# Kernel optimization log

Hardware: AMD Instinct MI355X
Metric: run time of the kernel (lower is better)

## Reference

```python
import jax, jax.numpy as jnp
import numpy as np

MARGIN = 0.1
PD_EPS = 1e-6  # torch.nn.PairwiseDistance default eps (added to the difference)

B = 4096
D = 512


def setup_inputs() -> dict:
    key = jax.random.key(0)
    k1, k2, k3 = jax.random.split(key, 3)
    return {
        "feature_ts": jax.random.normal(k1, (B, D), dtype=jnp.float32),
        "feature_image1": jax.random.normal(k2, (B, D), dtype=jnp.float32),
        "feature_image2": jax.random.normal(k3, (B, D), dtype=jnp.float32),
    }


def _safe_sqrt(sq):
    # sqrt with zero gradient at 0 (matches torch.cdist backward at zero distance)
    pos = sq > 0
    return jnp.where(pos, jnp.sqrt(jnp.where(pos, sq, 1.0)), 0.0)


def reference(feature_ts, feature_image1, feature_image2):
    b, d = feature_ts.shape
    # representations: [3B, D]
    reps = jnp.concatenate([feature_ts, feature_image1, feature_image2], axis=0)

    # cdist(feature_ts, reps, p=2) -> [B, 3B] via Gram-matrix expansion
    sq = (
        jnp.sum(feature_ts * feature_ts, axis=1)[:, None]
        + jnp.sum(reps * reps, axis=1)[None, :]
        - 2.0 * (feature_ts @ reps.T)
    )
    dist = _safe_sqrt(jnp.maximum(sq, 0.0))          # [B, 3B]
    dist = jax.nn.relu(dist)                          # faithful (no-op: dist >= 0)

    # PairwiseDistance(p=2): ||x1 - x2 + eps||_2
    diff = feature_image1 - feature_image2 + PD_EPS
    dist12 = jnp.sqrt(jnp.sum(diff * diff, axis=1))   # [B]

    idx = jnp.arange(b)
    l_pos_1 = dist[idx, idx + b]                      # diag offset B
    l_pos_2 = dist[idx, idx + 2 * b]                  # diag offset 2B

    positives = l_pos_1 + l_pos_2 + dist12            # [B]
    positive_value = jnp.maximum(l_pos_1, l_pos_2)    # [B]

    # negatives: all columns except {i, i+B, i+2B}; masked min instead of gather
    cols = jnp.arange(3 * b)[None, :]
    rows = idx[:, None]
    same = (cols == rows) | (cols == rows + b) | (cols == rows + 2 * b)
    negative_value = jnp.min(jnp.where(same, jnp.inf, dist), axis=1)  # [B]

    triplet = jax.nn.relu(positives - negative_value + MARGIN) + positive_value
    return jnp.sum(triplet) / b
```

## Files before the change

kernel.cpp:

```cpp
#include <hip/hip_runtime.h>
#include <hip/hip_bf16.h>

typedef unsigned short u16;
typedef unsigned int u32;
typedef __attribute__((ext_vector_type(8))) short bf16x8;
typedef __attribute__((ext_vector_type(4))) float f32x4;

#define NB 4096
#define ND 512
#define NREPS (3*NB)
#define BM 128
#define BN 256
#define BK 64
#define NKT (ND/BK)
#define ASZ (BM*BK)
#define BSZ (BN*BK)

#define GLD16(gp, lp)                                                         \
  __builtin_amdgcn_global_load_lds(                                           \
      (const __attribute__((address_space(1))) void*)(gp),                    \
      (__attribute__((address_space(3))) void*)(lp), 16, 0, 0)

__device__ __forceinline__ u16 f2bf(float f) {
  union { float f; u32 u; } v; v.f = f;
  u32 u = v.u;
  u32 r = (u + 0x7FFFu + ((u >> 16) & 1u)) >> 16;
  return (u16)r;
}

__global__ __launch_bounds__(256) void prep_all(
    const float* __restrict__ ts, const float* __restrict__ i1,
    const float* __restrict__ i2, u16* __restrict__ reps,
    float* __restrict__ norms, float* __restrict__ dist12,
    u32* __restrict__ minsq)
{
  __shared__ float s1[ND], s2[ND];
  const int r = blockIdx.x;
  const int tid = threadIdx.x;
  const int wave = tid >> 6, lane = tid & 63;

  if (wave < 3) {
    const float* src = (wave == 0) ? ts + (size_t)r * ND
                     : (wave == 1) ? i1 + (size_t)r * ND
                     :               i2 + (size_t)r * ND;
    const float4* s4 = (const float4*)src;
    float4 a = s4[lane*2+0];
    float4 b = s4[lane*2+1];
    if (wave == 1) { ((float4*)s1)[lane*2+0] = a; ((float4*)s1)[lane*2+1] = b; }
    if (wave == 2) { ((float4*)s2)[lane*2+0] = a; ((float4*)s2)[lane*2+1] = b; }
    float ss = a.x*a.x + a.y*a.y + a.z*a.z + a.w*a.w
             + b.x*b.x + b.y*b.y + b.z*b.z + b.w*b.w;
    uint4 pk;
    pk.x = (u32)f2bf(a.x) | ((u32)f2bf(a.y) << 16);
    pk.y = (u32)f2bf(a.z) | ((u32)f2bf(a.w) << 16);
    pk.z = (u32)f2bf(b.x) | ((u32)f2bf(b.y) << 16);
    pk.w = (u32)f2bf(b.z) | ((u32)f2bf(b.w) << 16);
    *(uint4*)(reps + (size_t)(wave*NB + r) * ND + lane*8) = pk;
    #pragma unroll
    for (int off = 32; off; off >>= 1) ss += __shfl_down(ss, off);
    if (lane == 0) norms[wave*NB + r] = ss;
  }
  __syncthreads();
  if (wave == 3) {
    float ss = 0.f;
    #pragma unroll
    for (int i = 0; i < 2; ++i) {
      float4 a = ((float4*)s1)[lane*2+i];
      float4 b = ((float4*)s2)[lane*2+i];
      float d0 = a.x - b.x + 1e-6f, d1 = a.y - b.y + 1e-6f;
      float d2 = a.z - b.z + 1e-6f, d3 = a.w - b.w + 1e-6f;
      ss += d0*d0 + d1*d1 + d2*d2 + d3*d3;
    }
    #pragma unroll
    for (int off = 32; off; off >>= 1) ss += __shfl_down(ss, off);
    if (lane == 0) { dist12[r] = sqrtf(ss); minsq[r] = 0x7F800000u; }
  }
}

__global__ __launch_bounds__(512) void gemm_min(
    const u16* __restrict__ reps, const float* __restrict__ norms,
    u32* __restrict__ minsq, float* __restrict__ lpos1,
    float* __restrict__ lpos2)
{
  __shared__ u16 As[ASZ];
  __shared__ u16 Bs[BSZ];
  const int tid  = threadIdx.x;
  const int lane = tid & 63;
  const int wave = tid >> 6;
  const int wr = wave >> 2;
  const int wc = wave & 3;
  const int fr = lane & 15, fg = lane >> 4;

  const int rowBase = blockIdx.x * BM;
  const int colBase = blockIdx.y * BN;

  const int rloc = lane >> 3;
  const int sp   = lane & 7;
  const u16* srcA[2]; u16* dstA[2];
  const u16* srcB[4]; u16* dstB[4];
  #pragma unroll
  for (int i = 0; i < 2; ++i) {
    const int r = wave*16 + i*8 + rloc;
    const int g = sp ^ (r & 7);
    srcA[i] = reps + (size_t)(rowBase + r) * ND + g*8;
    dstA[i] = &As[(wave*16 + i*8) * BK];
  }
  #pragma unroll
  for (int i = 0; i < 4; ++i) {
    const int r = wave*32 + i*8 + rloc;
    const int g = sp ^ (r & 7);
    srcB[i] = reps + (size_t)(colBase + r) * ND + g*8;
    dstB[i] = &Bs[(wave*32 + i*8) * BK];
  }

  f32x4 acc[4][4];
  const f32x4 zero = {0.f, 0.f, 0.f, 0.f};
  #pragma unroll
  for (int i = 0; i < 4; ++i)
    #pragma unroll
    for (int j = 0; j < 4; ++j)
      acc[i][j] = zero;

  for (int kt = 0; kt < NKT; ++kt) {
    const int koff = kt * BK;
    #pragma unroll
    for (int i = 0; i < 2; ++i) GLD16(srcA[i] + koff, dstA[i]);
    #pragma unroll
    for (int i = 0; i < 4; ++i) GLD16(srcB[i] + koff, dstB[i]);
    __syncthreads();

    bf16x8 af[4][2], bfr[4][2];
    #pragma unroll
    for (int mf = 0; mf < 4; ++mf)
      #pragma unroll
      for (int ks = 0; ks < 2; ++ks) {
        const int rowA = wr*64 + mf*16 + fr;
        const int slot = ks*4 + fg;
        af[mf][ks]  = *(const bf16x8*)&As[rowA*BK + (slot ^ (rowA & 7))*8];
        const int rowB = wc*64 + mf*16 + fr;
        bfr[mf][ks] = *(const bf16x8*)&Bs[rowB*BK + (slot ^ (rowB & 7))*8];
      }
    #pragma unroll
    for (int ks = 0; ks < 2; ++ks)
      #pragma unroll
      for (int mf = 0; mf < 4; ++mf)
        #pragma unroll
        for (int nf = 0; nf < 4; ++nf)
          acc[mf][nf] = __builtin_amdgcn_mfma_f32_16x16x32_bf16(
              af[mf][ks], bfr[nf][ks], acc[mf][nf], 0, 0, 0);
    __syncthreads();
  }

  float ncol[4];
  #pragma unroll
  for (int nf = 0; nf < 4; ++nf)
    ncol[nf] = norms[colBase + wc*64 + nf*16 + fr];
  const float INF = __builtin_inff();
  #pragma unroll
  for (int mf = 0; mf < 4; ++mf) {
    #pragma unroll
    for (int q = 0; q < 4; ++q) {
      const int r_g = rowBase + wr*64 + mf*16 + fg*4 + q;
      const float ntr = norms[r_g];
      float vm = INF;
      #pragma unroll
      for (int nf = 0; nf < 4; ++nf) {
        const int c_g = colBase + wc*64 + nf*16 + fr;
        const float dot = acc[mf][nf][q];
        const float sq = ntr + ncol[nf] - 2.0f * dot;
        if (c_g == r_g + NB)   lpos1[r_g] = sq;
        if (c_g == r_g + 2*NB) lpos2[r_g] = sq;
        const bool excl = (c_g == r_g) || (c_g == r_g + NB) || (c_g == r_g + 2*NB);
        const float v = excl ? INF : fmaxf(sq, 0.0f);
        vm = fminf(vm, v);
      }
      #pragma unroll
      for (int off = 1; off < 16; off <<= 1)
        vm = fminf(vm, __shfl_xor(vm, off));
      if (fr == 0)
        atomicMin(minsq + r_g, __float_as_uint(vm));
    }
  }
}

__global__ __launch_bounds__(1024) void finalize(
    const float* __restrict__ lpos1, const float* __restrict__ lpos2,
    const float* __restrict__ dist12, const u32* __restrict__ minsq,
    float* __restrict__ out)
{
  __shared__ float red[16];
  const int tid = threadIdx.x;
  float s = 0.f;
  for (int r = tid; r < NB; r += 1024) {
    float l1 = sqrtf(fmaxf(lpos1[r], 0.f));
    float l2 = sqrtf(fmaxf(lpos2[r], 0.f));
    float neg = sqrtf(__uint_as_float(minsq[r]));
    float pos = l1 + l2 + dist12[r];
    s += fmaxf(pos - neg + 0.1f, 0.f) + fmaxf(l1, l2);
  }
  #pragma unroll
  for (int off = 32; off; off >>= 1) s += __shfl_down(s, off);
  if ((tid & 63) == 0) red[tid >> 6] = s;
  __syncthreads();
  if (tid == 0) {
    float t = 0.f;
    #pragma unroll
    for (int i = 0; i < 16; ++i) t += red[i];
    out[0] = t * (1.0f / NB);
  }
}

extern "C" void kernel_launch(void* const* d_in, const int* in_sizes, int n_in,
                              void* d_out, int out_size, void* d_ws, size_t ws_size,
                              hipStream_t stream) {
  const float* ts = (const float*)d_in[0];
  const float* i1 = (const float*)d_in[1];
  const float* i2 = (const float*)d_in[2];
  float* out = (float*)d_out;

  char* p = (char*)d_ws;
  u16* reps    = (u16*)p;            p += (size_t)NREPS * ND * sizeof(u16);
  float* norms = (float*)p;          p += (size_t)NREPS * sizeof(float);
  float* dist12 = (float*)p;         p += (size_t)NB * sizeof(float);
  u32* minsq   = (u32*)p;            p += (size_t)NB * sizeof(u32);
  float* lpos1 = (float*)p;          p += (size_t)NB * sizeof(float);
  float* lpos2 = (float*)p;          p += (size_t)NB * sizeof(float);

  prep_all<<<NB, 256, 0, stream>>>(ts, i1, i2, reps, norms, dist12, minsq);
  dim3 grid(NB / BM, NREPS / BN);
  gemm_min<<<grid, 512, 0, stream>>>(reps, norms, minsq, lpos1, lpos2);
  finalize<<<1, 1024, 0, stream>>>(lpos1, lpos2, dist12, minsq, out);
}
```

Before: 144.2 us.

## Switch Gram GEMM to FP8 e4m3 with scaled 32x32x64 MFMA

Representations are quantized to FP8 e4m3 instead of bf16, and the GEMM uses the MI355X scaled f8f6f4 32x32x64 MFMA with unit scales. The K tile is doubled and the epilogue is reworked for the 32x32 accumulator layout with 32-lane min reductions. This halves operand bytes and raises MFMA throughput, at the cost of much coarser precision in the distance values, which could shift the min-negative selection and the loss.

```diff
diff --git a/kernel.cpp b/kernel.cpp
--- a/kernel.cpp
+++ b/kernel.cpp
@@ -1,36 +1,38 @@
 #include <hip/hip_runtime.h>
 #include <hip/hip_bf16.h>
-
+#include <hip/hip_fp8.h>
+
+typedef unsigned char u8;
 typedef unsigned short u16;
 typedef unsigned int u32;
-typedef __attribute__((ext_vector_type(8))) short bf16x8;
-typedef __attribute__((ext_vector_type(4))) float f32x4;
+typedef __attribute__((ext_vector_type(4))) int i32x4;
+typedef __attribute__((ext_vector_type(8))) int i32x8;
+typedef __attribute__((ext_vector_type(16))) float f32x16;
 
 #define NB 4096
 #define ND 512
 #define NREPS (3*NB)
 #define BM 128
 #define BN 256
-#define BK 64
+#define BK 128
 #define NKT (ND/BK)
 #define ASZ (BM*BK)
 #define BSZ (BN*BK)
+#define SCL 0x7F7F7F7F
 
 #define GLD16(gp, lp)                                                         \
   __builtin_amdgcn_global_load_lds(                                           \
       (const __attribute__((address_space(1))) void*)(gp),                    \
       (__attribute__((address_space(3))) void*)(lp), 16, 0, 0)
 
-__device__ __forceinline__ u16 f2bf(float f) {
-  union { float f; u32 u; } v; v.f = f;
-  u32 u = v.u;
-  u32 r = (u + 0x7FFFu + ((u >> 16) & 1u)) >> 16;
-  return (u16)r;
+__device__ __forceinline__ u32 pk4(float a, float b, float c, float d) {
+  __hip_fp8_e4m3 qa(a), qb(b), qc(c), qd(d);
+  return (u32)qa.__x | ((u32)qb.__x << 8) | ((u32)qc.__x << 16) | ((u32)qd.__x << 24);
 }
 
 __global__ __launch_bounds__(256) void prep_all(
     const float* __restrict__ ts, const float* __restrict__ i1,
-    const float* __restrict__ i2, u16* __restrict__ reps,
+    const float* __restrict__ i2, u8* __restrict__ reps,
     float* __restrict__ norms, float* __restrict__ dist12,
     u32* __restrict__ minsq)
 {
@@ -50,12 +52,10 @@
     if (wave == 2) { ((float4*)s2)[lane*2+0] = a; ((float4*)s2)[lane*2+1] = b; }
     float ss = a.x*a.x + a.y*a.y + a.z*a.z + a.w*a.w
              + b.x*b.x + b.y*b.y + b.z*b.z + b.w*b.w;
-    uint4 pk;
-    pk.x = (u32)f2bf(a.x) | ((u32)f2bf(a.y) << 16);
-    pk.y = (u32)f2bf(a.z) | ((u32)f2bf(a.w) << 16);
-    pk.z = (u32)f2bf(b.x) | ((u32)f2bf(b.y) << 16);
-    pk.w = (u32)f2bf(b.z) | ((u32)f2bf(b.w) << 16);
-    *(uint4*)(reps + (size_t)(wave*NB + r) * ND + lane*8) = pk;
+    uint2 pk;
+    pk.x = pk4(a.x, a.y, a.z, a.w);
+    pk.y = pk4(b.x, b.y, b.z, b.w);
+    *(uint2*)(reps + (size_t)(wave*NB + r) * ND + lane*8) = pk;
     #pragma unroll
     for (int off = 32; off; off >>= 1) ss += __shfl_down(ss, off);
     if (lane == 0) norms[wave*NB + r] = ss;
@@ -77,49 +77,58 @@
   }
 }
 
-__global__ __launch_bounds__(512) void gemm_min(
-    const u16* __restrict__ reps, const float* __restrict__ norms,
+__device__ __forceinline__ i32x8 rd_op(const u8* __restrict__ S, int row,
+                                       int ks, int hi) {
+  const int sw = row & 7;
+  const int s0 = ks*4 + hi*2;
+  const i32x4 lo = *(const i32x4*)&S[row*BK + ((s0 ^ sw) << 4)];
+  const i32x4 h  = *(const i32x4*)&S[row*BK + (((s0+1) ^ sw) << 4)];
+  i32x8 r;
+  r[0]=lo[0]; r[1]=lo[1]; r[2]=lo[2]; r[3]=lo[3];
+  r[4]=h[0];  r[5]=h[1];  r[6]=h[2];  r[7]=h[3];
+  return r;
+}
+
+#define MFMA8(a,b,c) __builtin_amdgcn_mfma_scale_f32_32x32x64_f8f6f4(          \
+    (a), (b), (c), 0, 0, 0, SCL, 0, SCL)
+
+__global__ __launch_bounds__(512, 4) void gemm_min(
+    const u8* __restrict__ reps, const float* __restrict__ norms,
     u32* __restrict__ minsq, float* __restrict__ lpos1,
     float* __restrict__ lpos2)
 {
-  __shared__ u16 As[ASZ];
-  __shared__ u16 Bs[BSZ];
+  __shared__ u8 As[ASZ];
+  __shared__ u8 Bs[BSZ];
   const int tid  = threadIdx.x;
   const int lane = tid & 63;
   const int wave = tid >> 6;
   const int wr = wave >> 2;
   const int wc = wave & 3;
-  const int fr = lane & 15, fg = lane >> 4;
+  const int lc = lane & 31;
+  const int hi = lane >> 5;
 
   const int rowBase = blockIdx.x * BM;
   const int colBase = blockIdx.y * BN;
 
   const int rloc = lane >> 3;
   const int sp   = lane & 7;
-  const u16* srcA[2]; u16* dstA[2];
-  const u16* srcB[4]; u16* dstB[4];
+  const int g    = sp ^ rloc;
+  const u8* srcA[2]; u8* dstA[2];
+  const u8* srcB[4]; u8* dstB[4];
   #pragma unroll
   for (int i = 0; i < 2; ++i) {
     const int r = wave*16 + i*8 + rloc;
-    const int g = sp ^ (r & 7);
-    srcA[i] = reps + (size_t)(rowBase + r) * ND + g*8;
+    srcA[i] = reps + (size_t)(rowBase + r) * ND + g*16;
     dstA[i] = &As[(wave*16 + i*8) * BK];
   }
   #pragma unroll
   for (int i = 0; i < 4; ++i) {
     const int r = wave*32 + i*8 + rloc;
-    const int g = sp ^ (r & 7);
-    srcB[i] = reps + (size_t)(colBase + r) * ND + g*8;
+    srcB[i] = reps + (size_t)(colBase + r) * ND + g*16;
     dstB[i] = &Bs[(wave*32 + i*8) * BK];
   }
 
-  f32x4 acc[4][4];
-  const f32x4 zero = {0.f, 0.f, 0.f, 0.f};
-  #pragma unroll
-  for (int i = 0; i < 4; ++i)
-    #pragma unroll
-    for (int j = 0; j < 4; ++j)
-      acc[i][j] = zero;
+  f32x16 acc00 = {}, acc01 = {}, acc10 = {}, acc11 = {};
 
   for (int kt = 0; kt < NKT; ++kt) {
     const int koff = kt * BK;
@@ -129,58 +138,50 @@
     for (int i = 0; i < 4; ++i) GLD16(srcB[i] + koff, dstB[i]);
     __syncthreads();
 
-    bf16x8 af[4][2], bfr[4][2];
-    #pragma unroll
-    for (int mf = 0; mf < 4; ++mf)
-      #pragma unroll
-      for (int ks = 0; ks < 2; ++ks) {
-        const int rowA = wr*64 + mf*16 + fr;
-        const int slot = ks*4 + fg;
-        af[mf][ks]  = *(const bf16x8*)&As[rowA*BK + (slot ^ (rowA & 7))*8];
-        const int rowB = wc*64 + mf*16 + fr;
-        bfr[mf][ks] = *(const bf16x8*)&Bs[rowB*BK + (slot ^ (rowB & 7))*8];
-      }
-    #pragma unroll
-    for (int ks = 0; ks < 2; ++ks)
-      #pragma unroll
-      for (int mf = 0; mf < 4; ++mf)
-        #pragma unroll
-        for (int nf = 0; nf < 4; ++nf)
-          acc[mf][nf] = __builtin_amdgcn_mfma_f32_16x16x32_bf16(
-              af[mf][ks], bfr[nf][ks], acc[mf][nf], 0, 0, 0);
+    #pragma unroll
+    for (int ks = 0; ks < 2; ++ks) {
+      const i32x8 a0 = rd_op(As, wr*64      + lc, ks, hi);
+      const i32x8 a1 = rd_op(As, wr*64 + 32 + lc, ks, hi);
+      const i32x8 b0 = rd_op(Bs, wc*64      + lc, ks, hi);
+      const i32x8 b1 = rd_op(Bs, wc*64 + 32 + lc, ks, hi);
+      acc00 = MFMA8(a0, b0, acc00);
+      acc01 = MFMA8(a0, b1, acc01);
+      acc10 = MFMA8(a1, b0, acc10);
+      acc11 = MFMA8(a1, b1, acc11);
+    }
     __syncthreads();
   }
 
-  float ncol[4];
-  #pragma unroll
-  for (int nf = 0; nf < 4; ++nf)
-    ncol[nf] = norms[colBase + wc*64 + nf*16 + fr];
+  const float nc0 = norms[colBase + wc*64      + lc];
+  const float nc1 = norms[colBase + wc*64 + 32 + lc];
+  const int   c0g = colBase + wc*64      + lc;
+  const int   c1g = colBase + wc*64 + 32 + lc;
   const float INF = __builtin_inff();
-  #pragma unroll
-  for (int mf = 0; mf < 4; ++mf) {
-    #pragma unroll
-    for (int q = 0; q < 4; ++q) {
-      const int r_g = rowBase + wr*64 + mf*16 + fg*4 + q;
-      const float ntr = norms[r_g];
-      float vm = INF;
-      #pragma unroll
-      for (int nf = 0; nf < 4; ++nf) {
-        const int c_g = colBase + wc*64 + nf*16 + fr;
-        const float dot = acc[mf][nf][q];
-        const float sq = ntr + ncol[nf] - 2.0f * dot;
-        if (c_g == r_g + NB)   lpos1[r_g] = sq;
-        if (c_g == r_g + 2*NB) lpos2[r_g] = sq;
-        const bool excl = (c_g == r_g) || (c_g == r_g + NB) || (c_g == r_g + 2*NB);
-        const float v = excl ? INF : fmaxf(sq, 0.0f);
-        vm = fminf(vm, v);
-      }
-      #pragma unroll
-      for (int off = 1; off < 16; off <<= 1)
-        vm = fminf(vm, __shfl_xor(vm, off));
-      if (fr == 0)
-        atomicMin(minsq + r_g, __float_as_uint(vm));
-    }
-  }
+
+#define EPI(MI, ACCA, ACCB)                                                   \
+  { _Pragma("unroll")                                                         \
+    for (int reg = 0; reg < 16; ++reg) {                                      \
+      const int r_g = rowBase + wr*64 + (MI)*32 + (reg&3) + 8*(reg>>2) + 4*hi;\
+      const float ntr = norms[r_g];                                           \
+      const float sq0 = ntr + nc0 - 2.0f * (ACCA)[reg];                       \
+      const float sq1 = ntr + nc1 - 2.0f * (ACCB)[reg];                       \
+      if (c0g == r_g + NB)   lpos1[r_g] = sq0;                                \
+      if (c0g == r_g + 2*NB) lpos2[r_g] = sq0;                                \
+      if (c1g == r_g + NB)   lpos1[r_g] = sq1;                                \
+      if (c1g == r_g + 2*NB) lpos2[r_g] = sq1;                                \
+      const bool e0 = (c0g == r_g) || (c0g == r_g+NB) || (c0g == r_g+2*NB);   \
+      const bool e1 = (c1g == r_g) || (c1g == r_g+NB) || (c1g == r_g+2*NB);   \
+      float vm = fminf(e0 ? INF : fmaxf(sq0, 0.0f),                           \
+                       e1 ? INF : fmaxf(sq1, 0.0f));                          \
+      _Pragma("unroll")                                                       \
+      for (int off = 1; off < 32; off <<= 1)                                  \
+        vm = fminf(vm, __shfl_xor(vm, off));                                  \
+      if (lc == 0)                                                            \
+        atomicMin(minsq + r_g, __float_as_uint(vm));                          \
+    } }
+
+  EPI(0, acc00, acc01);
+  EPI(1, acc10, acc11);
 }
 
 __global__ __launch_bounds__(1024) void finalize(
@@ -219,7 +220,7 @@
   float* out = (float*)d_out;
 
   char* p = (char*)d_ws;
-  u16* reps    = (u16*)p;            p += (size_t)NREPS * ND * sizeof(u16);
+  u8* reps     = (u8*)p;             p += (size_t)NREPS * ND * sizeof(u8);
   float* norms = (float*)p;          p += (size_t)NREPS * sizeof(float);
   float* dist12 = (float*)p;         p += (size_t)NB * sizeof(float);
   u32* minsq   = (u32*)p;            p += (size_t)NB * sizeof(u32);
```

Result: slower. 233.3 us (+61.8%).

## Exploit symmetry of ts-ts distance block and drop LDS staging in prep

Applied to the files above, without the earlier changes.

The ts×ts part of the distance matrix is symmetric, so tiles strictly above the block diagonal exit early. Lower-triangle tiles now also reduce per-column minima and atomically update the row minimum of the transposed index, which covers the skipped tiles. Separately, the prep kernel's fourth wave reads image1/image2 rows straight from global memory instead of going through shared memory and a barrier. This removes about one sixth of the GEMM tiles, at the cost of extra column reductions and atomics on the remaining ts tiles.

```diff
diff --git a/kernel.cpp b/kernel.cpp
--- a/kernel.cpp
+++ b/kernel.cpp
@@ -34,7 +34,6 @@
     float* __restrict__ norms, float* __restrict__ dist12,
     u32* __restrict__ minsq)
 {
-  __shared__ float s1[ND], s2[ND];
   const int r = blockIdx.x;
   const int tid = threadIdx.x;
   const int wave = tid >> 6, lane = tid & 63;
@@ -46,8 +45,6 @@
     const float4* s4 = (const float4*)src;
     float4 a = s4[lane*2+0];
     float4 b = s4[lane*2+1];
-    if (wave == 1) { ((float4*)s1)[lane*2+0] = a; ((float4*)s1)[lane*2+1] = b; }
-    if (wave == 2) { ((float4*)s2)[lane*2+0] = a; ((float4*)s2)[lane*2+1] = b; }
     float ss = a.x*a.x + a.y*a.y + a.z*a.z + a.w*a.w
              + b.x*b.x + b.y*b.y + b.z*b.z + b.w*b.w;
     uint4 pk;
@@ -59,14 +56,13 @@
     #pragma unroll
     for (int off = 32; off; off >>= 1) ss += __shfl_down(ss, off);
     if (lane == 0) norms[wave*NB + r] = ss;
-  }
-  __syncthreads();
-  if (wave == 3) {
+  } else {
+    const float4* a4 = (const float4*)(i1 + (size_t)r * ND);
+    const float4* b4 = (const float4*)(i2 + (size_t)r * ND);
     float ss = 0.f;
     #pragma unroll
     for (int i = 0; i < 2; ++i) {
-      float4 a = ((float4*)s1)[lane*2+i];
-      float4 b = ((float4*)s2)[lane*2+i];
+      float4 a = a4[lane*2+i], b = b4[lane*2+i];
       float d0 = a.x - b.x + 1e-6f, d1 = a.y - b.y + 1e-6f;
       float d2 = a.z - b.z + 1e-6f, d3 = a.w - b.w + 1e-6f;
       ss += d0*d0 + d1*d1 + d2*d2 + d3*d3;
@@ -82,6 +78,12 @@
     u32* __restrict__ minsq, float* __restrict__ lpos1,
     float* __restrict__ lpos2)
 {
+  const int mx = blockIdx.x, ny = blockIdx.y;
+  const int rowBase = mx * BM;
+  const int colBase = ny * BN;
+  const bool tsTile = (colBase < NB);
+  if (tsTile && 2*ny > mx) return;
+
   __shared__ u16 As[ASZ];
   __shared__ u16 Bs[BSZ];
   const int tid  = threadIdx.x;
@@ -91,9 +93,6 @@
   const int wc = wave & 3;
   const int fr = lane & 15, fg = lane >> 4;
 
-  const int rowBase = blockIdx.x * BM;
-  const int colBase = blockIdx.y * BN;
-
   const int rloc = lane >> 3;
   const int sp   = lane & 7;
   const u16* srcA[2]; u16* dstA[2];
@@ -156,6 +155,8 @@
   for (int nf = 0; nf < 4; ++nf)
     ncol[nf] = norms[colBase + wc*64 + nf*16 + fr];
   const float INF = __builtin_inff();
+  float cmin[4] = {INF, INF, INF, INF};
+
   #pragma unroll
   for (int mf = 0; mf < 4; ++mf) {
     #pragma unroll
@@ -173,12 +174,26 @@
         const bool excl = (c_g == r_g) || (c_g == r_g + NB) || (c_g == r_g + 2*NB);
         const float v = excl ? INF : fmaxf(sq, 0.0f);
         vm = fminf(vm, v);
+        cmin[nf] = fminf(cmin[nf], v);
       }
       #pragma unroll
       for (int off = 1; off < 16; off <<= 1)
         vm = fminf(vm, __shfl_xor(vm, off));
       if (fr == 0)
         atomicMin(minsq + r_g, __float_as_uint(vm));
+    }
+  }
+
+  if (tsTile) {
+    #pragma unroll
+    for (int nf = 0; nf < 4; ++nf) {
+      float cm = cmin[nf];
+      cm = fminf(cm, __shfl_xor(cm, 16));
+      cm = fminf(cm, __shfl_xor(cm, 32));
+      if (fg == 0) {
+        const int c_g = colBase + wc*64 + nf*16 + fr;
+        atomicMin(minsq + c_g, __float_as_uint(cm));
+      }
     }
   }
 }
```

New measurement: 150.7 us. +4.5%, slower.
